# Optimization experiments

Hardware: AMD Instinct MI355X
Metric: run time of the kernel (lower is better)

Reference implementation:

```python
import jax, jax.numpy as jnp
import numpy as np

BN_EPS = 1e-3  # O-CNN default bn_eps
N_NODES = 150000
C_IN, C_OUT, K = 32, 64, 27  # 3x3x3 octree stencil


def setup_inputs() -> dict:
    key = jax.random.key(0)
    k1, k2, k3 = jax.random.split(key, 3)
    data_in = jax.random.normal(k1, (1, C_IN, N_NODES, 1), dtype=jnp.float32)
    # neighbor table: index == N_NODES marks an empty (zero) neighbor
    neigh = jax.random.randint(k2, (N_NODES, K), 0, N_NODES + 1, dtype=jnp.int32)
    W = jax.random.normal(k3, (C_OUT, C_IN, K), dtype=jnp.float32) * 0.05
    gamma = jnp.ones((C_OUT,), dtype=jnp.float32)
    beta = jnp.zeros((C_OUT,), dtype=jnp.float32)
    return {"data_in": data_in, "neigh": neigh, "W": W, "gamma": gamma, "beta": beta}


def reference(data_in, neigh, W, gamma, beta):
    # data_in: [1, C_in, N, 1] (O-CNN octree feature layout)
    x = data_in[0, :, :, 0]                                  # [C_in, N]
    # pad one zero column so neighbor index == N gathers zeros (empty octant)
    x_pad = jnp.concatenate([x, jnp.zeros((x.shape[0], 1), x.dtype)], axis=1)
    g = x_pad[:, neigh]                                      # [C_in, N, K] im2col gather
    y = jnp.einsum('oik,ink->on', W, g)                      # [C_out, N] GEMM
    # BatchNorm2d (training mode): stats per channel over all nodes, biased var
    mean = jnp.mean(y, axis=1, keepdims=True)
    var = jnp.mean(jnp.square(y - mean), axis=1, keepdims=True)
    yn = (y - mean) * jax.lax.rsqrt(var + BN_EPS)
    out = jnp.maximum(yn * gamma[:, None] + beta[:, None], 0.0)  # affine + ReLU
    return out[None, :, :, None]                             # [1, C_out, N, 1]
```

## Files before the change

kernel.cpp:

```cpp
#include <hip/hip_runtime.h>
#include <hip/hip_bf16.h>
#include <stdint.h>

#define N_NODES 150000
#define C_IN 32
#define C_OUT 64
#define K_TAPS 27
#define PF 3
#define NSLOTS 32

typedef __attribute__((ext_vector_type(8))) __bf16 bf16x8;
typedef __attribute__((ext_vector_type(4))) float f32x4;

__device__ __forceinline__ ushort f2bf(float f) {
    union { float f; uint32_t u; } v; v.f = f;
    uint32_t u = v.u;
    return (ushort)((u + 0x7FFFu + ((u >> 16) & 1u)) >> 16);
}

__global__ __launch_bounds__(256) void k_transpose(const float* __restrict__ x,
                                                   ushort* __restrict__ xT) {
    __shared__ float tile[32][65];
    int t = threadIdx.x;
    int nb = blockIdx.x * 64;
    int nl = t & 63, i4 = t >> 6;
#pragma unroll
    for (int rep = 0; rep < 8; ++rep) {
        int i = rep * 4 + i4;
        int n = nb + nl;
        tile[i][nl] = (n < N_NODES) ? x[(size_t)i * N_NODES + n] : 0.0f;
    }
    __syncthreads();
    int nr = t >> 2, c0 = (t & 3) * 8;
    int n = nb + nr;
    if (n <= N_NODES) {
        uint32_t w[4];
#pragma unroll
        for (int j = 0; j < 4; ++j) {
            ushort lo = f2bf(tile[c0 + 2 * j][nr]);
            ushort hi = f2bf(tile[c0 + 2 * j + 1][nr]);
            w[j] = (uint32_t)lo | ((uint32_t)hi << 16);
        }
        *reinterpret_cast<uint4*>(xT + (size_t)n * 32 + c0) =
            make_uint4(w[0], w[1], w[2], w[3]);
    }
}

__global__ __launch_bounds__(256) void k_prep_w(const float* __restrict__ W,
                                                ushort* __restrict__ A_frag,
                                                float* __restrict__ stats) {
    int tid = blockIdx.x * 256 + threadIdx.x;
    if (tid < NSLOTS * 128 + 128) stats[tid] = 0.0f;
    if (tid < C_OUT * C_IN * K_TAPS) {
        int j = tid & 7;
        int ln = (tid >> 3) & 63;
        int km = tid >> 9;
        int m = km & 3;
        int k = km >> 2;
        int o = m * 16 + (ln & 15);
        int i = (ln >> 4) * 8 + j;
        A_frag[tid] = f2bf(W[o * (C_IN * K_TAPS) + i * K_TAPS + k]);
    }
}

__global__ __launch_bounds__(64, 4) void k_conv(const ushort* __restrict__ xT,
                                                const ushort* __restrict__ A_frag,
                                                const int* __restrict__ neigh,
                                                float* __restrict__ y,
                                                float* __restrict__ stats) {
    __shared__ int soff[32 * K_TAPS];
    int t = threadIdx.x;
    int nb = blockIdx.x * 32;
    for (int j = t; j < 32 * K_TAPS; j += 64) {
        int ng = nb + j / K_TAPS;
        int idx = (ng < N_NODES) ? neigh[(size_t)nb * K_TAPS + j] : N_NODES;
        soff[j] = idx << 6;
    }
    __syncthreads();

    int l15 = t & 15, quad = t >> 4;
    int qoff = quad << 4;

    const char* xTb = (const char*)xT;
    const char* aB = (const char*)A_frag + (size_t)t * 16;

    f32x4 acc[4][2];
#pragma unroll
    for (int m = 0; m < 4; ++m)
#pragma unroll
        for (int g = 0; g < 2; ++g) acc[m][g] = (f32x4){0.f, 0.f, 0.f, 0.f};

    bf16x8 bb[PF][2], aa[PF][4];

#pragma unroll
    for (int s = 0; s < PF; ++s) {
#pragma unroll
        for (int g = 0; g < 2; ++g)
            bb[s][g] = *reinterpret_cast<const bf16x8*>(
                xTb + (uint32_t)soff[(g * 16 + l15) * K_TAPS + s] + qoff);
#pragma unroll
        for (int m = 0; m < 4; ++m)
            aa[s][m] = *reinterpret_cast<const bf16x8*>(aB + ((size_t)(s * 4 + m) << 10));
    }

#pragma unroll 3
    for (int k = 0; k < K_TAPS; ++k) {
        int cur = k % PF;
#pragma unroll
        for (int m = 0; m < 4; ++m)
#pragma unroll
            for (int g = 0; g < 2; ++g)
                acc[m][g] = __builtin_amdgcn_mfma_f32_16x16x32_bf16(
                    aa[cur][m], bb[cur][g], acc[m][g], 0, 0, 0);
        if (k < K_TAPS - PF) {
            int kn = k + PF;
#pragma unroll
            for (int g = 0; g < 2; ++g)
                bb[cur][g] = *reinterpret_cast<const bf16x8*>(
                    xTb + (uint32_t)soff[(g * 16 + l15) * K_TAPS + kn] + qoff);
#pragma unroll
            for (int m = 0; m < 4; ++m)
                aa[cur][m] = *reinterpret_cast<const bf16x8*>(
                    aB + ((size_t)(kn * 4 + m) << 10));
        }
    }

#pragma unroll
    for (int m = 0; m < 4; ++m) {
        int obase = m * 16 + quad * 4;
#pragma unroll
        for (int g = 0; g < 2; ++g) {
            int n = nb + g * 16 + l15;
            if (n < N_NODES) {
#pragma unroll
                for (int r = 0; r < 4; ++r)
                    y[(size_t)(obase + r) * N_NODES + n] = acc[m][g][r];
            }
        }
    }

    int slot = blockIdx.x & (NSLOTS - 1);
#pragma unroll
    for (int m = 0; m < 4; ++m) {
#pragma unroll
        for (int r = 0; r < 4; ++r) {
            float s = 0.f, sq = 0.f;
#pragma unroll
            for (int g = 0; g < 2; ++g) {
                float v = acc[m][g][r];
                s += v;
                sq += v * v;
            }
#pragma unroll
            for (int d = 1; d < 16; d <<= 1) {
                s += __shfl_xor(s, d);
                sq += __shfl_xor(sq, d);
            }
            if (l15 == 0) {
                int o = m * 16 + quad * 4 + r;
                atomicAdd(&stats[slot * 128 + o], s);
                atomicAdd(&stats[slot * 128 + 64 + o], sq);
            }
        }
    }
}

__global__ void k_finalize(const float* __restrict__ stats, float* __restrict__ ss,
                           const float* __restrict__ gamma,
                           const float* __restrict__ beta) {
    int o = threadIdx.x;
    if (o < C_OUT) {
        float s = 0.f, sq = 0.f;
        for (int c = 0; c < NSLOTS; ++c) {
            s += stats[c * 128 + o];
            sq += stats[c * 128 + 64 + o];
        }
        const float invN = 1.0f / (float)N_NODES;
        float mean = s * invN;
        float var = sq * invN - mean * mean;
        float rstd = rsqrtf(var + 1e-3f);
        float sc = gamma[o] * rstd;
        ss[o] = sc;
        ss[C_OUT + o] = beta[o] - mean * sc;
    }
}

__global__ __launch_bounds__(256) void k_bn_relu(float* __restrict__ y,
                                                 const float* __restrict__ ss) {
    int o = blockIdx.y;
    int i = blockIdx.x * 256 + threadIdx.x;
    float sc = ss[o], sh = ss[C_OUT + o];
    if (i < N_NODES / 4) {
        float4* p = reinterpret_cast<float4*>(y + (size_t)o * N_NODES) + i;
        float4 v = *p;
        v.x = fmaxf(fmaf(v.x, sc, sh), 0.f);
        v.y = fmaxf(fmaf(v.y, sc, sh), 0.f);
        v.z = fmaxf(fmaf(v.z, sc, sh), 0.f);
        v.w = fmaxf(fmaf(v.w, sc, sh), 0.f);
        *p = v;
    }
}

extern "C" void kernel_launch(void* const* d_in, const int* in_sizes, int n_in,
                              void* d_out, int out_size, void* d_ws, size_t ws_size,
                              hipStream_t stream) {
    const float* data_in = (const float*)d_in[0];
    const int* neigh = (const int*)d_in[1];
    const float* W = (const float*)d_in[2];
    const float* gamma = (const float*)d_in[3];
    const float* beta = (const float*)d_in[4];
    float* out = (float*)d_out;

    char* ws = (char*)d_ws;
    ushort* xT = (ushort*)ws;
    ushort* A_frag = (ushort*)(ws + 9601024);
    float* stats = (float*)(ws + 9711616);
    float* ss = stats + NSLOTS * 128;

    k_transpose<<<2344, 256, 0, stream>>>(data_in, xT);
    k_prep_w<<<(C_OUT * C_IN * K_TAPS + 255) / 256, 256, 0, stream>>>(W, A_frag, stats);
    k_conv<<<(N_NODES + 31) / 32, 64, 0, stream>>>(xT, A_frag, neigh, out, stats);
    k_finalize<<<1, 64, 0, stream>>>(stats, ss, gamma, beta);
    k_bn_relu<<<dim3((N_NODES / 4 + 255) / 256, C_OUT), 256, 0, stream>>>(out, ss);
}
```

Baseline: 184.9 us.

## Merge prep kernels, fold BN finalize into bn_relu, use 4-wave conv blocks

Combines the input transpose and the weight-fragment preparation into a single launch that dispatches on block index. The per-channel finalize is folded into the BN+ReLU kernel: each block reduces the 32 stat slots with shuffles and then handles four float4s per thread. The conv kernel now runs 256-thread blocks of four independent waves sharing one neighbor-offset staging pass, with a different occupancy hint. The aim is fewer launches and inter-kernel gaps, at the cost of redundant stat reductions per BN block and different register/LDS occupancy in conv.

New measurement: 311.8 us. 68.6% more time.

```diff
diff --git a/kernel.cpp b/kernel.cpp
--- a/kernel.cpp
+++ b/kernel.cpp
@@ -9,6 +9,10 @@
 #define PF 3
 #define NSLOTS 32
 
+#define TRANS_BLOCKS 2344
+#define WPREP_BLOCKS 216
+#define CONV_BLOCKS 1172
+
 typedef __attribute__((ext_vector_type(8))) __bf16 bf16x8;
 typedef __attribute__((ext_vector_type(4))) float f32x4;
 
@@ -18,71 +22,76 @@
     return (ushort)((u + 0x7FFFu + ((u >> 16) & 1u)) >> 16);
 }
 
-__global__ __launch_bounds__(256) void k_transpose(const float* __restrict__ x,
-                                                   ushort* __restrict__ xT) {
-    __shared__ float tile[32][65];
+__global__ __launch_bounds__(256) void k_prep(const float* __restrict__ x,
+                                              ushort* __restrict__ xT,
+                                              const float* __restrict__ W,
+                                              ushort* __restrict__ A_frag,
+                                              float* __restrict__ stats) {
     int t = threadIdx.x;
-    int nb = blockIdx.x * 64;
-    int nl = t & 63, i4 = t >> 6;
-#pragma unroll
-    for (int rep = 0; rep < 8; ++rep) {
-        int i = rep * 4 + i4;
-        int n = nb + nl;
-        tile[i][nl] = (n < N_NODES) ? x[(size_t)i * N_NODES + n] : 0.0f;
+    int b = blockIdx.x;
+    if (b < TRANS_BLOCKS) {
+        __shared__ float tile[32][65];
+        int nb = b * 64;
+        int nl = t & 63, i4 = t >> 6;
+#pragma unroll
+        for (int rep = 0; rep < 8; ++rep) {
+            int i = rep * 4 + i4;
+            int n = nb + nl;
+            tile[i][nl] = (n < N_NODES) ? x[(size_t)i * N_NODES + n] : 0.0f;
+        }
+        __syncthreads();
+        int nr = t >> 2, c0 = (t & 3) * 8;
+        int n = nb + nr;
+        if (n <= N_NODES) {
+            uint32_t w[4];
+#pragma unroll
+            for (int j = 0; j < 4; ++j) {
+                ushort lo = f2bf(tile[c0 + 2 * j][nr]);
+                ushort hi = f2bf(tile[c0 + 2 * j + 1][nr]);
+                w[j] = (uint32_t)lo | ((uint32_t)hi << 16);
+            }
+            *reinterpret_cast<uint4*>(xT + (size_t)n * 32 + c0) =
+                make_uint4(w[0], w[1], w[2], w[3]);
+        }
+    } else {
+        int tid = (b - TRANS_BLOCKS) * 256 + t;
+        if (tid < NSLOTS * 128 + 128) stats[tid] = 0.0f;
+        if (tid < C_OUT * C_IN * K_TAPS) {
+            int j = tid & 7;
+            int ln = (tid >> 3) & 63;
+            int km = tid >> 9;
+            int m = km & 3;
+            int k = km >> 2;
+            int o = m * 16 + (ln & 15);
+            int i = (ln >> 4) * 8 + j;
+            A_frag[tid] = f2bf(W[o * (C_IN * K_TAPS) + i * K_TAPS + k]);
+        }
+    }
+}
+
+__global__ __launch_bounds__(256, 6) void k_conv(const ushort* __restrict__ xT,
+                                                 const ushort* __restrict__ A_frag,
+                                                 const int* __restrict__ neigh,
+                                                 float* __restrict__ y,
+                                                 float* __restrict__ stats) {
+    __shared__ int soff[128 * K_TAPS];
+    int t = threadIdx.x;
+    int nblk = blockIdx.x * 128;
+    for (int j = t; j < 128 * K_TAPS; j += 256) {
+        int ng = nblk + j / K_TAPS;
+        int idx = (ng < N_NODES) ? neigh[(size_t)nblk * K_TAPS + j] : N_NODES;
+        soff[j] = idx << 6;
     }
     __syncthreads();
-    int nr = t >> 2, c0 = (t & 3) * 8;
-    int n = nb + nr;
-    if (n <= N_NODES) {
-        uint32_t w[4];
-#pragma unroll
-        for (int j = 0; j < 4; ++j) {
-            ushort lo = f2bf(tile[c0 + 2 * j][nr]);
-            ushort hi = f2bf(tile[c0 + 2 * j + 1][nr]);
-            w[j] = (uint32_t)lo | ((uint32_t)hi << 16);
-        }
-        *reinterpret_cast<uint4*>(xT + (size_t)n * 32 + c0) =
-            make_uint4(w[0], w[1], w[2], w[3]);
-    }
-}
-
-__global__ __launch_bounds__(256) void k_prep_w(const float* __restrict__ W,
-                                                ushort* __restrict__ A_frag,
-                                                float* __restrict__ stats) {
-    int tid = blockIdx.x * 256 + threadIdx.x;
-    if (tid < NSLOTS * 128 + 128) stats[tid] = 0.0f;
-    if (tid < C_OUT * C_IN * K_TAPS) {
-        int j = tid & 7;
-        int ln = (tid >> 3) & 63;
-        int km = tid >> 9;
-        int m = km & 3;
-        int k = km >> 2;
-        int o = m * 16 + (ln & 15);
-        int i = (ln >> 4) * 8 + j;
-        A_frag[tid] = f2bf(W[o * (C_IN * K_TAPS) + i * K_TAPS + k]);
-    }
-}
-
-__global__ __launch_bounds__(64, 4) void k_conv(const ushort* __restrict__ xT,
-                                                const ushort* __restrict__ A_frag,
-                                                const int* __restrict__ neigh,
-                                                float* __restrict__ y,
-                                                float* __restrict__ stats) {
-    __shared__ int soff[32 * K_TAPS];
-    int t = threadIdx.x;
-    int nb = blockIdx.x * 32;
-    for (int j = t; j < 32 * K_TAPS; j += 64) {
-        int ng = nb + j / K_TAPS;
-        int idx = (ng < N_NODES) ? neigh[(size_t)nb * K_TAPS + j] : N_NODES;
-        soff[j] = idx << 6;
-    }
-    __syncthreads();
-
-    int l15 = t & 15, quad = t >> 4;
+
+    int wid = t >> 6, lane = t & 63;
+    int l15 = lane & 15, quad = lane >> 4;
     int qoff = quad << 4;
+    int nb = nblk + wid * 32;
 
     const char* xTb = (const char*)xT;
-    const char* aB = (const char*)A_frag + (size_t)t * 16;
+    const char* aB = (const char*)A_frag + (size_t)lane * 16;
+    const int* so = soff + wid * 32 * K_TAPS;
 
     f32x4 acc[4][2];
 #pragma unroll
@@ -91,13 +100,12 @@
         for (int g = 0; g < 2; ++g) acc[m][g] = (f32x4){0.f, 0.f, 0.f, 0.f};
 
     bf16x8 bb[PF][2], aa[PF][4];
-
 #pragma unroll
     for (int s = 0; s < PF; ++s) {
 #pragma unroll
         for (int g = 0; g < 2; ++g)
             bb[s][g] = *reinterpret_cast<const bf16x8*>(
-                xTb + (uint32_t)soff[(g * 16 + l15) * K_TAPS + s] + qoff);
+                xTb + (uint32_t)so[(g * 16 + l15) * K_TAPS + s] + qoff);
 #pragma unroll
         for (int m = 0; m < 4; ++m)
             aa[s][m] = *reinterpret_cast<const bf16x8*>(aB + ((size_t)(s * 4 + m) << 10));
@@ -117,7 +125,7 @@
 #pragma unroll
             for (int g = 0; g < 2; ++g)
                 bb[cur][g] = *reinterpret_cast<const bf16x8*>(
-                    xTb + (uint32_t)soff[(g * 16 + l15) * K_TAPS + kn] + qoff);
+                    xTb + (uint32_t)so[(g * 16 + l15) * K_TAPS + kn] + qoff);
 #pragma unroll
             for (int m = 0; m < 4; ++m)
                 aa[cur][m] = *reinterpret_cast<const bf16x8*>(
@@ -165,39 +173,46 @@
     }
 }
 
-__global__ void k_finalize(const float* __restrict__ stats, float* __restrict__ ss,
-                           const float* __restrict__ gamma,
-                           const float* __restrict__ beta) {
-    int o = threadIdx.x;
-    if (o < C_OUT) {
-        float s = 0.f, sq = 0.f;
-        for (int c = 0; c < NSLOTS; ++c) {
-            s += stats[c * 128 + o];
-            sq += stats[c * 128 + 64 + o];
-        }
-        const float invN = 1.0f / (float)N_NODES;
-        float mean = s * invN;
-        float var = sq * invN - mean * mean;
-        float rstd = rsqrtf(var + 1e-3f);
-        float sc = gamma[o] * rstd;
-        ss[o] = sc;
-        ss[C_OUT + o] = beta[o] - mean * sc;
-    }
-}
-
 __global__ __launch_bounds__(256) void k_bn_relu(float* __restrict__ y,
-                                                 const float* __restrict__ ss) {
+                                                 const float* __restrict__ stats,
+                                                 const float* __restrict__ gamma,
+                                                 const float* __restrict__ beta) {
+    __shared__ float s_sc, s_sh;
+    int t = threadIdx.x;
     int o = blockIdx.y;
-    int i = blockIdx.x * 256 + threadIdx.x;
-    float sc = ss[o], sh = ss[C_OUT + o];
-    if (i < N_NODES / 4) {
-        float4* p = reinterpret_cast<float4*>(y + (size_t)o * N_NODES) + i;
-        float4 v = *p;
-        v.x = fmaxf(fmaf(v.x, sc, sh), 0.f);
-        v.y = fmaxf(fmaf(v.y, sc, sh), 0.f);
-        v.z = fmaxf(fmaf(v.z, sc, sh), 0.f);
-        v.w = fmaxf(fmaf(v.w, sc, sh), 0.f);
-        *p = v;
+    if (t < 32) {
+        float s = stats[t * 128 + o];
+        float sq = stats[t * 128 + 64 + o];
+#pragma unroll
+        for (int d = 1; d < 32; d <<= 1) {
+            s += __shfl_xor(s, d);
+            sq += __shfl_xor(sq, d);
+        }
+        if (t == 0) {
+            const float invN = 1.0f / (float)N_NODES;
+            float mean = s * invN;
+            float var = sq * invN - mean * mean;
+            float rstd = rsqrtf(var + 1e-3f);
+            float sc = gamma[o] * rstd;
+            s_sc = sc;
+            s_sh = beta[o] - mean * sc;
+        }
+    }
+    __syncthreads();
+    float sc = s_sc, sh = s_sh;
+    float4* row = reinterpret_cast<float4*>(y + (size_t)o * N_NODES);
+    int base = blockIdx.x * 1024 + t;
+#pragma unroll
+    for (int it = 0; it < 4; ++it) {
+        int i = base + it * 256;
+        if (i < N_NODES / 4) {
+            float4 v = row[i];
+            v.x = fmaxf(fmaf(v.x, sc, sh), 0.f);
+            v.y = fmaxf(fmaf(v.y, sc, sh), 0.f);
+            v.z = fmaxf(fmaf(v.z, sc, sh), 0.f);
+            v.w = fmaxf(fmaf(v.w, sc, sh), 0.f);
+            row[i] = v;
+        }
     }
 }
 
@@ -215,11 +230,10 @@
     ushort* xT = (ushort*)ws;
     ushort* A_frag = (ushort*)(ws + 9601024);
     float* stats = (float*)(ws + 9711616);
-    float* ss = stats + NSLOTS * 128;
-
-    k_transpose<<<2344, 256, 0, stream>>>(data_in, xT);
-    k_prep_w<<<(C_OUT * C_IN * K_TAPS + 255) / 256, 256, 0, stream>>>(W, A_frag, stats);
-    k_conv<<<(N_NODES + 31) / 32, 64, 0, stream>>>(xT, A_frag, neigh, out, stats);
-    k_finalize<<<1, 64, 0, stream>>>(stats, ss, gamma, beta);
-    k_bn_relu<<<dim3((N_NODES / 4 + 255) / 256, C_OUT), 256, 0, stream>>>(out, ss);
-}
+
+    k_prep<<<TRANS_BLOCKS + WPREP_BLOCKS, 256, 0, stream>>>(data_in, xT, W, A_frag,
+                                                            stats);
+    k_conv<<<CONV_BLOCKS, 256, 0, stream>>>(xT, A_frag, neigh, out, stats);
+    k_bn_relu<<<dim3((N_NODES / 4 + 1023) / 1024, C_OUT), 256, 0, stream>>>(
+        out, stats, gamma, beta);
+}
```
